# Performance work log

Hardware: AMD Instinct MI355X
Metric: run time of the kernel (lower is better)

Reference implementation:

```python
import jax, jax.numpy as jnp
import numpy as np

B, S, D_MODEL = 2, 2048, 2048
N_HEADS, D_HEAD = 32, 64
SEQ_MAX = 2048


def _rope_cache(seq_len, d_head):
    half = d_head // 2
    inv_freq = 1.0 / (10000.0 ** (np.arange(0, half, dtype=np.float32) / half))
    t = np.arange(seq_len, dtype=np.float32)
    freqs = np.einsum('i,j->ij', t, inv_freq)  # [S, half]
    emb = np.concatenate([freqs, freqs], axis=-1)  # [S, d_head]
    return jnp.asarray(np.cos(emb)), jnp.asarray(np.sin(emb))


def _rotate_half(x):
    half = x.shape[-1] // 2
    return jnp.concatenate([-x[..., half:], x[..., :half]], axis=-1)


def setup_inputs() -> dict:
    key = jax.random.key(0)
    ks = jax.random.split(key, 9)
    std = 0.02
    mk = lambda k: jax.random.normal(k, (D_MODEL, D_MODEL), jnp.float32) * std
    return {
        'x': jax.random.normal(ks[0], (B, S, D_MODEL), jnp.float32),
        'Wq': mk(ks[1]), 'bq': jnp.zeros((D_MODEL,), jnp.float32),
        'Wk': mk(ks[2]), 'bk': jnp.zeros((D_MODEL,), jnp.float32),
        'Wv': mk(ks[3]), 'bv': jnp.zeros((D_MODEL,), jnp.float32),
        'Wo': mk(ks[4]), 'bo': jnp.zeros((D_MODEL,), jnp.float32),
    }


def reference(x, Wq, bq, Wk, bk, Wv, bv, Wo, bo):
    Bsz, S_len, _ = x.shape
    # projections (torch Linear: y = x @ W^T + b)
    q = x @ Wq.T + bq
    k = x @ Wk.T + bk
    v = x @ Wv.T + bv
    # [B, H, S, Dh]
    to_heads = lambda t: t.reshape(Bsz, S_len, N_HEADS, D_HEAD).transpose(0, 2, 1, 3)
    q, k, v = to_heads(q), to_heads(k), to_heads(v)
    cos, sin = _rope_cache(S_len, D_HEAD)  # [S, Dh]
    cos = cos[None, None]
    sin = sin[None, None]
    q = q * cos + _rotate_half(q) * sin
    k = k * cos + _rotate_half(k) * sin
    scale = 1.0 / jnp.sqrt(jnp.float32(D_HEAD))
    att = jnp.einsum('bhqd,bhkd->bhqk', q, k) * scale
    causal = jnp.tril(jnp.ones((S_len, S_len), dtype=bool))
    att = jnp.where(causal[None, None], att, jnp.float32(-jnp.inf))
    att = jax.nn.softmax(att, axis=-1)
    # sigmoid-gated values (dropout = identity at inference)
    y = jnp.einsum('bhqk,bhkd->bhqd', att, jax.nn.sigmoid(v))
    y = y.transpose(0, 2, 1, 3).reshape(Bsz, S_len, D_MODEL)
    return y @ Wo.T + bo
```

## Files before the change

kernel.cpp:

```cpp
#include <hip/hip_runtime.h>

typedef unsigned short u16;
typedef float f32x4 __attribute__((ext_vector_type(4)));
typedef __bf16 bf16x8 __attribute__((ext_vector_type(8)));

#define S_LEN 2048
#define DM 2048
#define NHEAD 32
#define DHEAD 64

__device__ __forceinline__ u16 f2bf(float f) {
    __bf16 b = (__bf16)f;
    return __builtin_bit_cast(u16, b);
}
__device__ __forceinline__ float bf2f(u16 u) {
    return (float)__builtin_bit_cast(__bf16, u);
}
__device__ __forceinline__ void async16(const void* g, void* l) {
    __builtin_amdgcn_global_load_lds(
        (const __attribute__((address_space(1))) unsigned int*)g,
        (__attribute__((address_space(3))) unsigned int*)l, 16, 0, 0);
}
__device__ __forceinline__ void fast_sincos(float th, float* s, float* c) {
    float rev = th * 0.15915494309189535f;
    rev = rev - floorf(rev);
    *s = __builtin_amdgcn_sinf(rev);
    *c = __builtin_amdgcn_cosf(rev);
}
__device__ __forceinline__ float fexp2(float x) { return __builtin_amdgcn_exp2f(x); }

__global__ __launch_bounds__(256) void cast_all(const float* __restrict__ x,
                                                const float* __restrict__ Wq,
                                                const float* __restrict__ Wk,
                                                const float* __restrict__ Wv,
                                                const float* __restrict__ Wo,
                                                u16* __restrict__ xb,
                                                u16* __restrict__ Wqkv,
                                                u16* __restrict__ Wob) {
    int bid = blockIdx.x;
    const float* src;
    u16* dst;
    long long off;
    if (bid < 8192)       { src = x;  dst = xb;             off = (long long)bid * 1024; }
    else if (bid < 12288) { src = Wq; dst = Wqkv;           off = (long long)(bid - 8192) * 1024; }
    else if (bid < 16384) { src = Wk; dst = Wqkv + 4194304; off = (long long)(bid - 12288) * 1024; }
    else if (bid < 20480) { src = Wv; dst = Wqkv + 8388608; off = (long long)(bid - 16384) * 1024; }
    else                  { src = Wo; dst = Wob;            off = (long long)(bid - 20480) * 1024; }
    long long i = off + threadIdx.x * 4;
    float4 f = *(const float4*)(src + i);
    ushort4 v;
    v.x = f2bf(f.x); v.y = f2bf(f.y); v.z = f2bf(f.z); v.w = f2bf(f.w);
    *(ushort4*)(dst + i) = v;
}

__global__ __launch_bounds__(256) void rope_vsig(u16* __restrict__ Qb, u16* __restrict__ Kb,
                                                 const u16* __restrict__ V,
                                                 u16* __restrict__ VT) {
    int bid = blockIdx.x;
    if (bid < 32768) {
        long long idx = (long long)bid * 256 + threadIdx.x;
        int which = (int)(idx >> 22);
        int t = (int)(idx & 4194303);
        int j = t & 31;
        int h = (t >> 5) & 31;
        int row = t >> 10;
        int s = row & (S_LEN - 1);
        u16* T = which ? Kb : Qb;
        float scale = which ? 1.0f : 0.18033688011112042f;
        long long base = (long long)row * DM + h * DHEAD;
        float inv = __expf(-(float)j * 0.28782313662425575f);
        float sn, cs;
        fast_sincos((float)s * inv, &sn, &cs);
        float x1 = bf2f(T[base + j]);
        float x2 = bf2f(T[base + 32 + j]);
        T[base + j] = f2bf((x1 * cs - x2 * sn) * scale);
        T[base + 32 + j] = f2bf((x2 * cs + x1 * sn) * scale);
    } else {
        int vb = bid - 32768;
        int st = vb & 63;
        int h = vb >> 6;
        __shared__ u16 T[64][72];
        int r = threadIdx.x >> 2, c0 = (threadIdx.x & 3) * 16;
        const u16* src = V + (long long)(st * 64 + r) * DM + h * 64 + c0;
#pragma unroll
        for (int half = 0; half < 2; ++half) {
            bf16x8 v = *(const bf16x8*)(src + half * 8);
#pragma unroll
            for (int j = 0; j < 8; ++j) {
                float vf = (float)v[j];
                T[c0 + half * 8 + j][r] = f2bf(1.f / (1.f + __expf(-vf)));
            }
        }
        __syncthreads();
        int d = threadIdx.x >> 2, s0 = (threadIdx.x & 3) * 16;
        int b = st >> 5;
        int sl = (st & 31) * 64;
        u16* dst = VT + ((long long)((b * NHEAD + h) * DHEAD + d)) * S_LEN + sl + s0;
#pragma unroll
        for (int q = 0; q < 4; ++q)
            *(ushort4*)(dst + q * 4) = *(const ushort4*)(&T[d][s0] + q * 4);
    }
}

__global__ __launch_bounds__(256) void gemm_qkv(const u16* __restrict__ A,
                                                const u16* __restrict__ Bt,
                                                const float* __restrict__ bq,
                                                const float* __restrict__ bk,
                                                const float* __restrict__ bv,
                                                u16* __restrict__ Qo, u16* __restrict__ Ko,
                                                u16* __restrict__ Vo, int M, int K) {
    __shared__ __align__(16) u16 As[128 * 32];
    __shared__ __align__(16) u16 Bs[128 * 32];
    int tid = threadIdx.x;
    int w = tid >> 6, lane = tid & 63, quad = lane >> 4, l16 = lane & 15;
    int m0 = blockIdx.x * 128;
    int n0 = blockIdx.y * 128;
    int sel = n0 >> 11;
    int nloc = n0 & 2047;
    u16* out = sel == 0 ? Qo : (sel == 1 ? Ko : Vo);
    const float* bias = sel == 0 ? bq : (sel == 1 ? bk : bv);
    int wm = (w & 1) * 64, wn = (w >> 1) * 64;

    f32x4 acc[4][4] = {};
    const u16* ga = A + (long long)m0 * K;
    const u16* gb = Bt + (long long)n0 * K;

    for (int k0 = 0; k0 < K; k0 += 32) {
#pragma unroll
        for (int rr = 0; rr < 2; ++rr) {
            int c = tid + rr * 256;
            int row = c >> 2, kc = c & 3;
            async16(ga + (long long)row * K + k0 + kc * 8, (char*)As + c * 16);
            async16(gb + (long long)row * K + k0 + kc * 8, (char*)Bs + c * 16);
        }
        __syncthreads();
        bf16x8 af[4], bfv[4];
#pragma unroll
        for (int mt = 0; mt < 4; ++mt)
            af[mt] = *(const bf16x8*)(As + (wm + mt * 16 + l16) * 32 + quad * 8);
#pragma unroll
        for (int nt = 0; nt < 4; ++nt)
            bfv[nt] = *(const bf16x8*)(Bs + (wn + nt * 16 + l16) * 32 + quad * 8);
#pragma unroll
        for (int mt = 0; mt < 4; ++mt)
#pragma unroll
            for (int nt = 0; nt < 4; ++nt)
                acc[mt][nt] = __builtin_amdgcn_mfma_f32_16x16x32_bf16(af[mt], bfv[nt],
                                                                      acc[mt][nt], 0, 0, 0);
        __syncthreads();
    }

#pragma unroll
    for (int mt = 0; mt < 4; ++mt) {
#pragma unroll
        for (int nt = 0; nt < 4; ++nt) {
            int col = nloc + wn + nt * 16 + l16;
            float bvs = bias[col];
#pragma unroll
            for (int r = 0; r < 4; ++r) {
                int row = m0 + wm + mt * 16 + quad * 4 + r;
                out[(long long)row * 2048 + col] = f2bf(acc[mt][nt][r] + bvs);
            }
        }
    }
}

__global__ __launch_bounds__(256) void gemm_bt_f32(const u16* __restrict__ A,
                                                   const u16* __restrict__ Bt,
                                                   const float* __restrict__ bias,
                                                   float* __restrict__ Cout,
                                                   int M, int N, int K) {
    __shared__ __align__(16) u16 As[128 * 32];
    __shared__ __align__(16) u16 Bs[128 * 32];
    int tid = threadIdx.x;
    int w = tid >> 6, lane = tid & 63, quad = lane >> 4, l16 = lane & 15;
    int m0 = blockIdx.x * 128;
    int n0 = blockIdx.y * 128;
    int wm = (w & 1) * 64, wn = (w >> 1) * 64;

    f32x4 acc[4][4] = {};
    const u16* ga = A + (long long)m0 * K;
    const u16* gb = Bt + (long long)n0 * K;

    for (int k0 = 0; k0 < K; k0 += 32) {
#pragma unroll
        for (int rr = 0; rr < 2; ++rr) {
            int c = tid + rr * 256;
            int row = c >> 2, kc = c & 3;
            async16(ga + (long long)row * K + k0 + kc * 8, (char*)As + c * 16);
            async16(gb + (long long)row * K + k0 + kc * 8, (char*)Bs + c * 16);
        }
        __syncthreads();
        bf16x8 af[4], bfv[4];
#pragma unroll
        for (int mt = 0; mt < 4; ++mt)
            af[mt] = *(const bf16x8*)(As + (wm + mt * 16 + l16) * 32 + quad * 8);
#pragma unroll
        for (int nt = 0; nt < 4; ++nt)
            bfv[nt] = *(const bf16x8*)(Bs + (wn + nt * 16 + l16) * 32 + quad * 8);
#pragma unroll
        for (int mt = 0; mt < 4; ++mt)
#pragma unroll
            for (int nt = 0; nt < 4; ++nt)
                acc[mt][nt] = __builtin_amdgcn_mfma_f32_16x16x32_bf16(af[mt], bfv[nt],
                                                                      acc[mt][nt], 0, 0, 0);
        __syncthreads();
    }

#pragma unroll
    for (int mt = 0; mt < 4; ++mt) {
#pragma unroll
        for (int nt = 0; nt < 4; ++nt) {
            int col = n0 + wn + nt * 16 + l16;
            float bvs = bias[col];
#pragma unroll
            for (int r = 0; r < 4; ++r) {
                int row = m0 + wm + mt * 16 + quad * 4 + r;
                Cout[(long long)row * N + col] = acc[mt][nt][r] + bvs;
            }
        }
    }
}

__global__ __launch_bounds__(256, 2) void flash_attn(const u16* __restrict__ Q,
                                                     const u16* __restrict__ K,
                                                     const u16* __restrict__ VT,
                                                     u16* __restrict__ Y) {
    int bid = blockIdx.x;
    int xcd = bid & 7;
    int idx = bid >> 3;
    int pi = idx & 7;
    int hg = xcd * 8 + (idx >> 3);
    int b = hg >> 5, h = hg & 31;
    int tid = threadIdx.x;
    int w = tid >> 6, lane = tid & 63, quad = lane >> 4, l16 = lane & 15;

    __shared__ __align__(16) u16 Kl[2][64 * 64];
    __shared__ __align__(16) u16 Vl[2][64 * 64];
    __shared__ __align__(16) u16 Pl[4][32 * 64];

    const u16* kbase = K + ((long long)(b * S_LEN)) * DM + h * DHEAD;
    const u16* vbase = VT + ((long long)((b * NHEAD + h) * DHEAD)) * S_LEN;

    bf16x8 kpre[2], vpre[2];
    int c0 = tid, c1 = tid + 256;
    int row0 = c0 >> 3, lc0 = (c0 & 7) ^ (row0 & 7);
    int row1 = c1 >> 3, lc1 = (c1 & 7) ^ (row1 & 7);

    kpre[0] = *(const bf16x8*)(kbase + (long long)row0 * DM + lc0 * 8);
    vpre[0] = *(const bf16x8*)(vbase + (long long)row0 * S_LEN + lc0 * 8);
    kpre[1] = *(const bf16x8*)(kbase + (long long)row1 * DM + lc1 * 8);
    vpre[1] = *(const bf16x8*)(vbase + (long long)row1 * S_LEN + lc1 * 8);

    int it = 0;
#pragma unroll 1
    for (int rep = 0; rep < 2; ++rep) {
        int qt = rep ? 15 - pi : pi;
        bf16x8 aq[2][2];
#pragma unroll
        for (int sub = 0; sub < 2; ++sub) {
            int qrow = qt * 128 + w * 32 + sub * 16 + l16;
            const u16* qp = Q + ((long long)(b * S_LEN + qrow)) * DM + h * DHEAD + quad * 8;
            aq[sub][0] = *(const bf16x8*)(qp);
            aq[sub][1] = *(const bf16x8*)(qp + 32);
        }

        f32x4 o[2][4] = {};
        float m_r[2] = {-__builtin_inff(), -__builtin_inff()};
        float l_r[2] = {0.f, 0.f};

        int kts = 2 * qt + 2;
#pragma unroll 1
        for (int kt = 0; kt < kts; ++kt) {
            u16* Kb_ = Kl[it & 1];
            u16* Vb_ = Vl[it & 1];
            *(bf16x8*)((char*)Kb_ + c0 * 16) = kpre[0];
            *(bf16x8*)((char*)Vb_ + c0 * 16) = vpre[0];
            *(bf16x8*)((char*)Kb_ + c1 * 16) = kpre[1];
            *(bf16x8*)((char*)Vb_ + c1 * 16) = vpre[1];
            {
                int nk0 = (kt + 1 < kts ? kt + 1 : 0) * 64;
                kpre[0] = *(const bf16x8*)(kbase + (long long)(nk0 + row0) * DM + lc0 * 8);
                vpre[0] = *(const bf16x8*)(vbase + (long long)row0 * S_LEN + nk0 + lc0 * 8);
                kpre[1] = *(const bf16x8*)(kbase + (long long)(nk0 + row1) * DM + lc1 * 8);
                vpre[1] = *(const bf16x8*)(vbase + (long long)row1 * S_LEN + nk0 + lc1 * 8);
            }
            __syncthreads();

            bf16x8 ak0[4], ak1[4];
#pragma unroll
            for (int nt = 0; nt < 4; ++nt) {
                int row = nt * 16 + l16;
                ak0[nt] = *(const bf16x8*)(Kb_ + row * 64 + (quad ^ (row & 7)) * 8);
                ak1[nt] = *(const bf16x8*)(Kb_ + row * 64 + ((quad + 4) ^ (row & 7)) * 8);
            }

            bf16x8 bp[2][2];
            u16* pw = &Pl[w][0];
#pragma unroll
            for (int sub = 0; sub < 2; ++sub) {
                f32x4 s[4];
#pragma unroll
                for (int nt = 0; nt < 4; ++nt) {
                    f32x4 a = {};
                    a = __builtin_amdgcn_mfma_f32_16x16x32_bf16(ak0[nt], aq[sub][0], a, 0, 0, 0);
                    a = __builtin_amdgcn_mfma_f32_16x16x32_bf16(ak1[nt], aq[sub][1], a, 0, 0, 0);
                    s[nt] = a;
                }
                if (kt >= 2 * qt) {
                    int qg = qt * 128 + w * 32 + sub * 16 + l16;
#pragma unroll
                    for (int nt = 0; nt < 4; ++nt) {
#pragma unroll
                        for (int r = 0; r < 4; ++r) {
                            int kg = kt * 64 + nt * 16 + quad * 4 + r;
                            if (kg > qg) s[nt][r] = -__builtin_inff();
                        }
                    }
                }
                float mx = s[0][0];
#pragma unroll
                for (int nt = 0; nt < 4; ++nt)
#pragma unroll
                    for (int r = 0; r < 4; ++r) mx = fmaxf(mx, s[nt][r]);
                mx = fmaxf(mx, __shfl_xor(mx, 16, 64));
                mx = fmaxf(mx, __shfl_xor(mx, 32, 64));
                float mnew = fmaxf(m_r[sub], mx);
                float alpha = fexp2(m_r[sub] - mnew);
                m_r[sub] = mnew;
#pragma unroll
                for (int nt = 0; nt < 4; ++nt)
#pragma unroll
                    for (int r = 0; r < 4; ++r) s[nt][r] = fexp2(s[nt][r] - mnew);
                float sum = 0.f;
#pragma unroll
                for (int nt = 0; nt < 4; ++nt)
#pragma unroll
                    for (int r = 0; r < 4; ++r) sum += s[nt][r];
                sum += __shfl_xor(sum, 16, 64);
                sum += __shfl_xor(sum, 32, 64);
                l_r[sub] = l_r[sub] * alpha + sum;
#pragma unroll
                for (int dt = 0; dt < 4; ++dt)
#pragma unroll
                    for (int r = 0; r < 4; ++r) o[sub][dt][r] *= alpha;

                int prow = sub * 16 + l16;
#pragma unroll
                for (int nt = 0; nt < 4; ++nt) {
                    ushort4 pk;
                    pk.x = f2bf(s[nt][0]); pk.y = f2bf(s[nt][1]);
                    pk.z = f2bf(s[nt][2]); pk.w = f2bf(s[nt][3]);
                    int chunk = (nt * 2 + (quad >> 1)) ^ (l16 & 7);
                    *(ushort4*)(pw + prow * 64 + chunk * 8 + (quad & 1) * 4) = pk;
                }
                bp[sub][0] = *(const bf16x8*)(pw + prow * 64 + (quad ^ (l16 & 7)) * 8);
                bp[sub][1] = *(const bf16x8*)(pw + prow * 64 + ((quad + 4) ^ (l16 & 7)) * 8);
            }

#pragma unroll
            for (int dt = 0; dt < 4; ++dt) {
                int row = dt * 16 + l16;
                bf16x8 av0 = *(const bf16x8*)(Vb_ + row * 64 + (quad ^ (row & 7)) * 8);
                bf16x8 av1 = *(const bf16x8*)(Vb_ + row * 64 + ((quad + 4) ^ (row & 7)) * 8);
#pragma unroll
                for (int sub = 0; sub < 2; ++sub) {
                    o[sub][dt] = __builtin_amdgcn_mfma_f32_16x16x32_bf16(av0, bp[sub][0],
                                                                         o[sub][dt], 0, 0, 0);
                    o[sub][dt] = __builtin_amdgcn_mfma_f32_16x16x32_bf16(av1, bp[sub][1],
                                                                         o[sub][dt], 0, 0, 0);
                }
            }
            ++it;
        }

#pragma unroll
        for (int sub = 0; sub < 2; ++sub) {
            float inv_l = 1.f / l_r[sub];
            u16* yp = Y + ((long long)(b * S_LEN + qt * 128 + w * 32 + sub * 16 + l16)) * DM
                      + h * DHEAD;
#pragma unroll
            for (int dt = 0; dt < 4; ++dt) {
                ushort4 yk;
                yk.x = f2bf(o[sub][dt][0] * inv_l);
                yk.y = f2bf(o[sub][dt][1] * inv_l);
                yk.z = f2bf(o[sub][dt][2] * inv_l);
                yk.w = f2bf(o[sub][dt][3] * inv_l);
                *(ushort4*)(yp + dt * 16 + quad * 4) = yk;
            }
        }
    }
}

extern "C" void kernel_launch(void* const* d_in, const int* in_sizes, int n_in,
                              void* d_out, int out_size, void* d_ws, size_t ws_size,
                              hipStream_t stream) {
    const float* x  = (const float*)d_in[0];
    const float* Wq = (const float*)d_in[1];
    const float* bq = (const float*)d_in[2];
    const float* Wk = (const float*)d_in[3];
    const float* bk = (const float*)d_in[4];
    const float* Wv = (const float*)d_in[5];
    const float* bv = (const float*)d_in[6];
    const float* Wo = (const float*)d_in[7];
    const float* bo = (const float*)d_in[8];

    const long long M = 2LL * S_LEN;

    char* ws = (char*)d_ws;
    u16* xb   = (u16*)(ws);
    u16* Wqkv = (u16*)(ws + 16 * 1024 * 1024);
    u16* Wob  = (u16*)(ws + 40 * 1024 * 1024);
    u16* Qb   = (u16*)(ws + 48 * 1024 * 1024);
    u16* Kb   = (u16*)(ws + 64 * 1024 * 1024);
    u16* Vb   = (u16*)(ws + 80 * 1024 * 1024);
    u16* Yb   = (u16*)(ws + 96 * 1024 * 1024);
    u16* VTb  = (u16*)(ws + 112 * 1024 * 1024);

    cast_all<<<24576, 256, 0, stream>>>(x, Wq, Wk, Wv, Wo, xb, Wqkv, Wob);

    dim3 gqkv(32, 48);
    gemm_qkv<<<gqkv, 256, 0, stream>>>(xb, Wqkv, bq, bk, bv, Qb, Kb, Vb, (int)M, DM);

    rope_vsig<<<34816, 256, 0, stream>>>(Qb, Kb, Vb, VTb);

    flash_attn<<<2 * NHEAD * 8, 256, 0, stream>>>(Qb, Kb, VTb, Yb);

    dim3 gg(32, 16);
    gemm_bt_f32<<<gg, 256, 0, stream>>>(Yb, Wob, bo, (float*)d_out, (int)M, DM, DM);
}
```

Measured before the change: 416.0 us.

## Rewrite QKV GEMM as 256x256 double-buffered 8-wave pipelined kernel

Replaces the 128x128 single-buffered QKV projection GEMM with a 256x256-tile kernel using 8 waves and double-buffered LDS. The next K-tile is loaded asynchronously while MFMAs run, with explicit vmcnt/lgkmcnt waits and barriers, s_setprio around the MFMA bursts, and a remapped block order for L2 locality. The goal is to hide global load latency and raise arithmetic intensity per tile. In exchange it uses much more LDS (128KB) and more registers per block, which may limit occupancy, and correctness now depends on hand-placed waitcnt and barrier ordering.

```diff
diff --git a/kernel.cpp b/kernel.cpp
--- a/kernel.cpp
+++ b/kernel.cpp
@@ -102,64 +102,149 @@
     }
 }
 
-__global__ __launch_bounds__(256) void gemm_qkv(const u16* __restrict__ A,
-                                                const u16* __restrict__ Bt,
-                                                const float* __restrict__ bq,
-                                                const float* __restrict__ bk,
-                                                const float* __restrict__ bv,
-                                                u16* __restrict__ Qo, u16* __restrict__ Ko,
-                                                u16* __restrict__ Vo, int M, int K) {
-    __shared__ __align__(16) u16 As[128 * 32];
-    __shared__ __align__(16) u16 Bs[128 * 32];
+__global__ __launch_bounds__(512, 2) void gemm_qkv8(const u16* __restrict__ A,
+                                                    const u16* __restrict__ Bt,
+                                                    const float* __restrict__ bq,
+                                                    const float* __restrict__ bk,
+                                                    const float* __restrict__ bv,
+                                                    u16* __restrict__ Qo, u16* __restrict__ Ko,
+                                                    u16* __restrict__ Vo) {
+    constexpr int K = 2048;
+    constexpr int NT = 32;
+    __shared__ __align__(16) u16 As[2][2][256 * 32];
+    __shared__ __align__(16) u16 Bs[2][2][256 * 32];
+
     int tid = threadIdx.x;
     int w = tid >> 6, lane = tid & 63, quad = lane >> 4, l16 = lane & 15;
-    int m0 = blockIdx.x * 128;
-    int n0 = blockIdx.y * 128;
-    int sel = n0 >> 11;
-    int nloc = n0 & 2047;
+    int wm = (w >> 2) * 128;
+    int wn = (w & 3) * 64;
+
+    int bid = blockIdx.x;
+    int wgid = (bid & 7) * 48 + (bid >> 3);
+    int mtile = wgid & 15;
+    int ntile = wgid >> 4;
+
+    int m0 = mtile * 256;
+    int n0g = ntile * 256;
+    int sel = n0g >> 11;
+    int nloc = n0g & 2047;
     u16* out = sel == 0 ? Qo : (sel == 1 ? Ko : Vo);
     const float* bias = sel == 0 ? bq : (sel == 1 ? bk : bv);
-    int wm = (w & 1) * 64, wn = (w >> 1) * 64;
-
-    f32x4 acc[4][4] = {};
+
     const u16* ga = A + (long long)m0 * K;
-    const u16* gb = Bt + (long long)n0 * K;
-
-    for (int k0 = 0; k0 < K; k0 += 32) {
-#pragma unroll
-        for (int rr = 0; rr < 2; ++rr) {
-            int c = tid + rr * 256;
-            int row = c >> 2, kc = c & 3;
-            async16(ga + (long long)row * K + k0 + kc * 8, (char*)As + c * 16);
-            async16(gb + (long long)row * K + k0 + kc * 8, (char*)Bs + c * 16);
-        }
-        __syncthreads();
-        bf16x8 af[4], bfv[4];
+    const u16* gb = Bt + (long long)n0g * K;
+
+    auto stage = [&](const u16* gbase, int kt, int h, u16* plane) {
+#pragma unroll
+        for (int r = 0; r < 2; ++r) {
+            int off = (tid + r * 512) * 16;
+            int row = off >> 6;
+            int ce = (off & 63) >> 1;
+            async16(gbase + (long long)row * K + kt * 64 + h * 32 + ce,
+                    (char*)plane + off);
+        }
+    };
+
+    f32x4 acc[8][4] = {};
+    bf16x8 af[4], bfr[4];
+
+    auto rdA = [&](const u16* pA, int mh) {
 #pragma unroll
         for (int mt = 0; mt < 4; ++mt)
-            af[mt] = *(const bf16x8*)(As + (wm + mt * 16 + l16) * 32 + quad * 8);
+            af[mt] = *(const bf16x8*)(pA + (wm + mh * 64 + mt * 16 + l16) * 32 + quad * 8);
+    };
+    auto rdB = [&](const u16* pB) {
 #pragma unroll
         for (int nt = 0; nt < 4; ++nt)
-            bfv[nt] = *(const bf16x8*)(Bs + (wn + nt * 16 + l16) * 32 + quad * 8);
+            bfr[nt] = *(const bf16x8*)(pB + (wn + nt * 16 + l16) * 32 + quad * 8);
+    };
+    auto mm = [&](int mh) {
+        __builtin_amdgcn_s_setprio(1);
 #pragma unroll
         for (int mt = 0; mt < 4; ++mt)
 #pragma unroll
             for (int nt = 0; nt < 4; ++nt)
-                acc[mt][nt] = __builtin_amdgcn_mfma_f32_16x16x32_bf16(af[mt], bfv[nt],
-                                                                      acc[mt][nt], 0, 0, 0);
-        __syncthreads();
-    }
-
-#pragma unroll
-    for (int mt = 0; mt < 4; ++mt) {
+                acc[mh * 4 + mt][nt] = __builtin_amdgcn_mfma_f32_16x16x32_bf16(
+                    af[mt], bfr[nt], acc[mh * 4 + mt][nt], 0, 0, 0);
+        __builtin_amdgcn_s_setprio(0);
+    };
+
+    stage(ga, 0, 0, &As[0][0][0]);
+    stage(gb, 0, 0, &Bs[0][0][0]);
+    stage(ga, 0, 1, &As[0][1][0]);
+    stage(gb, 0, 1, &Bs[0][1][0]);
+    asm volatile("s_waitcnt vmcnt(4)" ::: "memory");
+    __builtin_amdgcn_s_barrier();
+
+#pragma unroll 1
+    for (int t = 0; t < NT - 1; ++t) {
+        int bf = t & 1, nb = bf ^ 1;
+        rdA(&As[bf][0][0], 0);
+        rdB(&Bs[bf][0][0]);
+        stage(ga, t + 1, 0, &As[nb][0][0]);
+        __builtin_amdgcn_s_barrier();
+        asm volatile("s_waitcnt lgkmcnt(0)" ::: "memory");
+        mm(0);
+        __builtin_amdgcn_s_barrier();
+        rdA(&As[bf][0][0], 1);
+        stage(gb, t + 1, 0, &Bs[nb][0][0]);
+        __builtin_amdgcn_s_barrier();
+        asm volatile("s_waitcnt lgkmcnt(0)" ::: "memory");
+        mm(1);
+        asm volatile("s_waitcnt vmcnt(4)" ::: "memory");
+        __builtin_amdgcn_s_barrier();
+        rdA(&As[bf][1][0], 0);
+        rdB(&Bs[bf][1][0]);
+        stage(ga, t + 1, 1, &As[nb][1][0]);
+        __builtin_amdgcn_s_barrier();
+        asm volatile("s_waitcnt lgkmcnt(0)" ::: "memory");
+        mm(0);
+        __builtin_amdgcn_s_barrier();
+        rdA(&As[bf][1][0], 1);
+        stage(gb, t + 1, 1, &Bs[nb][1][0]);
+        __builtin_amdgcn_s_barrier();
+        asm volatile("s_waitcnt lgkmcnt(0)" ::: "memory");
+        mm(1);
+        asm volatile("s_waitcnt vmcnt(4)" ::: "memory");
+        __builtin_amdgcn_s_barrier();
+    }
+    {
+        int bf = (NT - 1) & 1;
+        rdA(&As[bf][0][0], 0);
+        rdB(&Bs[bf][0][0]);
+        __builtin_amdgcn_s_barrier();
+        asm volatile("s_waitcnt lgkmcnt(0)" ::: "memory");
+        mm(0);
+        __builtin_amdgcn_s_barrier();
+        rdA(&As[bf][0][0], 1);
+        __builtin_amdgcn_s_barrier();
+        asm volatile("s_waitcnt lgkmcnt(0)" ::: "memory");
+        mm(1);
+        asm volatile("s_waitcnt vmcnt(0)" ::: "memory");
+        __builtin_amdgcn_s_barrier();
+        rdA(&As[bf][1][0], 0);
+        rdB(&Bs[bf][1][0]);
+        __builtin_amdgcn_s_barrier();
+        asm volatile("s_waitcnt lgkmcnt(0)" ::: "memory");
+        mm(0);
+        __builtin_amdgcn_s_barrier();
+        rdA(&As[bf][1][0], 1);
+        __builtin_amdgcn_s_barrier();
+        asm volatile("s_waitcnt lgkmcnt(0)" ::: "memory");
+        mm(1);
+        __builtin_amdgcn_s_barrier();
+    }
+
+#pragma unroll
+    for (int mf = 0; mf < 8; ++mf) {
 #pragma unroll
         for (int nt = 0; nt < 4; ++nt) {
             int col = nloc + wn + nt * 16 + l16;
             float bvs = bias[col];
 #pragma unroll
             for (int r = 0; r < 4; ++r) {
-                int row = m0 + wm + mt * 16 + quad * 4 + r;
-                out[(long long)row * 2048 + col] = f2bf(acc[mt][nt][r] + bvs);
+                int row = m0 + wm + mf * 16 + quad * 4 + r;
+                out[(long long)row * 2048 + col] = f2bf(acc[mf][nt][r] + bvs);
             }
         }
     }
@@ -419,8 +504,7 @@
 
     cast_all<<<24576, 256, 0, stream>>>(x, Wq, Wk, Wv, Wo, xb, Wqkv, Wob);
 
-    dim3 gqkv(32, 48);
-    gemm_qkv<<<gqkv, 256, 0, stream>>>(xb, Wqkv, bq, bk, bv, Qb, Kb, Vb, (int)M, DM);
+    gemm_qkv8<<<384, 512, 0, stream>>>(xb, Wqkv, bq, bk, bv, Qb, Kb, Vb);
 
     rope_vsig<<<34816, 256, 0, stream>>>(Qb, Kb, Vb, VTb);
 
```

Measured after the change: 436.9 us. 5.0% more time.

## Fuse RoPE, Q scaling, and V sigmoid-transpose into QKV GEMM epilogue

Applied to the files above, without the earlier changes.

Removes the separate rope_vsig kernel. The QKV GEMM epilogue now applies rotary embedding and the Q scale directly to the accumulators, pairing columns d and d+32 held by the same warp. It also writes sigmoid(V) transposed straight into the VT layout. This saves one kernel launch and a full read-modify-write pass over Q, K and V, at the cost of a heavier epilogue with sincos work and strided 8-byte stores for VT.

```diff
diff --git a/kernel.cpp b/kernel.cpp
--- a/kernel.cpp
+++ b/kernel.cpp
@@ -53,62 +53,13 @@
     *(ushort4*)(dst + i) = v;
 }
 
-__global__ __launch_bounds__(256) void rope_vsig(u16* __restrict__ Qb, u16* __restrict__ Kb,
-                                                 const u16* __restrict__ V,
-                                                 u16* __restrict__ VT) {
-    int bid = blockIdx.x;
-    if (bid < 32768) {
-        long long idx = (long long)bid * 256 + threadIdx.x;
-        int which = (int)(idx >> 22);
-        int t = (int)(idx & 4194303);
-        int j = t & 31;
-        int h = (t >> 5) & 31;
-        int row = t >> 10;
-        int s = row & (S_LEN - 1);
-        u16* T = which ? Kb : Qb;
-        float scale = which ? 1.0f : 0.18033688011112042f;
-        long long base = (long long)row * DM + h * DHEAD;
-        float inv = __expf(-(float)j * 0.28782313662425575f);
-        float sn, cs;
-        fast_sincos((float)s * inv, &sn, &cs);
-        float x1 = bf2f(T[base + j]);
-        float x2 = bf2f(T[base + 32 + j]);
-        T[base + j] = f2bf((x1 * cs - x2 * sn) * scale);
-        T[base + 32 + j] = f2bf((x2 * cs + x1 * sn) * scale);
-    } else {
-        int vb = bid - 32768;
-        int st = vb & 63;
-        int h = vb >> 6;
-        __shared__ u16 T[64][72];
-        int r = threadIdx.x >> 2, c0 = (threadIdx.x & 3) * 16;
-        const u16* src = V + (long long)(st * 64 + r) * DM + h * 64 + c0;
-#pragma unroll
-        for (int half = 0; half < 2; ++half) {
-            bf16x8 v = *(const bf16x8*)(src + half * 8);
-#pragma unroll
-            for (int j = 0; j < 8; ++j) {
-                float vf = (float)v[j];
-                T[c0 + half * 8 + j][r] = f2bf(1.f / (1.f + __expf(-vf)));
-            }
-        }
-        __syncthreads();
-        int d = threadIdx.x >> 2, s0 = (threadIdx.x & 3) * 16;
-        int b = st >> 5;
-        int sl = (st & 31) * 64;
-        u16* dst = VT + ((long long)((b * NHEAD + h) * DHEAD + d)) * S_LEN + sl + s0;
-#pragma unroll
-        for (int q = 0; q < 4; ++q)
-            *(ushort4*)(dst + q * 4) = *(const ushort4*)(&T[d][s0] + q * 4);
-    }
-}
-
 __global__ __launch_bounds__(256) void gemm_qkv(const u16* __restrict__ A,
                                                 const u16* __restrict__ Bt,
                                                 const float* __restrict__ bq,
                                                 const float* __restrict__ bk,
                                                 const float* __restrict__ bv,
                                                 u16* __restrict__ Qo, u16* __restrict__ Ko,
-                                                u16* __restrict__ Vo, int M, int K) {
+                                                u16* __restrict__ VT, int M, int K) {
     __shared__ __align__(16) u16 As[128 * 32];
     __shared__ __align__(16) u16 Bs[128 * 32];
     int tid = threadIdx.x;
@@ -117,7 +68,6 @@
     int n0 = blockIdx.y * 128;
     int sel = n0 >> 11;
     int nloc = n0 & 2047;
-    u16* out = sel == 0 ? Qo : (sel == 1 ? Ko : Vo);
     const float* bias = sel == 0 ? bq : (sel == 1 ? bk : bv);
     int wm = (w & 1) * 64, wn = (w >> 1) * 64;
 
@@ -150,16 +100,48 @@
         __syncthreads();
     }
 
-#pragma unroll
-    for (int mt = 0; mt < 4; ++mt) {
-#pragma unroll
-        for (int nt = 0; nt < 4; ++nt) {
-            int col = nloc + wn + nt * 16 + l16;
-            float bvs = bias[col];
-#pragma unroll
-            for (int r = 0; r < 4; ++r) {
-                int row = m0 + wm + mt * 16 + quad * 4 + r;
-                out[(long long)row * 2048 + col] = f2bf(acc[mt][nt][r] + bvs);
+    if (sel < 2) {
+        u16* out = sel == 0 ? Qo : Ko;
+        float scale = sel == 0 ? 0.18033688011112042f : 1.0f;
+        float invf[2];
+        invf[0] = __expf(-(float)l16 * 0.28782313662425575f);
+        invf[1] = __expf(-(float)(16 + l16) * 0.28782313662425575f);
+#pragma unroll
+        for (int mt = 0; mt < 4; ++mt) {
+#pragma unroll
+            for (int nt = 0; nt < 2; ++nt) {
+                int col1 = nloc + wn + nt * 16 + l16;
+                int col2 = col1 + 32;
+                float b1 = bias[col1], b2 = bias[col2];
+#pragma unroll
+                for (int r = 0; r < 4; ++r) {
+                    int row = m0 + wm + mt * 16 + quad * 4 + r;
+                    int s = row & (S_LEN - 1);
+                    float sn, cs;
+                    fast_sincos((float)s * invf[nt], &sn, &cs);
+                    float x1 = acc[mt][nt][r] + b1;
+                    float x2 = acc[mt][nt + 2][r] + b2;
+                    out[(long long)row * 2048 + col1] = f2bf((x1 * cs - x2 * sn) * scale);
+                    out[(long long)row * 2048 + col2] = f2bf((x2 * cs + x1 * sn) * scale);
+                }
+            }
+        }
+    } else {
+#pragma unroll
+        for (int mt = 0; mt < 4; ++mt) {
+#pragma unroll
+            for (int nt = 0; nt < 4; ++nt) {
+                int col = nloc + wn + nt * 16 + l16;
+                int h = col >> 6, d = col & 63;
+                float bvs = bias[col];
+                int row0 = m0 + wm + mt * 16 + quad * 4;
+                int b = row0 >> 11, s0 = row0 & (S_LEN - 1);
+                ushort4 pk;
+                pk.x = f2bf(1.f / (1.f + __expf(-(acc[mt][nt][0] + bvs))));
+                pk.y = f2bf(1.f / (1.f + __expf(-(acc[mt][nt][1] + bvs))));
+                pk.z = f2bf(1.f / (1.f + __expf(-(acc[mt][nt][2] + bvs))));
+                pk.w = f2bf(1.f / (1.f + __expf(-(acc[mt][nt][3] + bvs))));
+                *(ushort4*)(VT + ((long long)((b * NHEAD + h) * DHEAD + d)) * S_LEN + s0) = pk;
             }
         }
     }
@@ -413,16 +395,13 @@
     u16* Wob  = (u16*)(ws + 40 * 1024 * 1024);
     u16* Qb   = (u16*)(ws + 48 * 1024 * 1024);
     u16* Kb   = (u16*)(ws + 64 * 1024 * 1024);
-    u16* Vb   = (u16*)(ws + 80 * 1024 * 1024);
     u16* Yb   = (u16*)(ws + 96 * 1024 * 1024);
     u16* VTb  = (u16*)(ws + 112 * 1024 * 1024);
 
     cast_all<<<24576, 256, 0, stream>>>(x, Wq, Wk, Wv, Wo, xb, Wqkv, Wob);
 
     dim3 gqkv(32, 48);
-    gemm_qkv<<<gqkv, 256, 0, stream>>>(xb, Wqkv, bq, bk, bv, Qb, Kb, Vb, (int)M, DM);
-
-    rope_vsig<<<34816, 256, 0, stream>>>(Qb, Kb, Vb, VTb);
+    gemm_qkv<<<gqkv, 256, 0, stream>>>(xb, Wqkv, bq, bk, bv, Qb, Kb, VTb, (int)M, DM);
 
     flash_attn<<<2 * NHEAD * 8, 256, 0, stream>>>(Qb, Kb, VTb, Yb);
 
```

New measurement: 424.4 us. +2.0%, slower.
